# Performance work log

Hardware: AMD Instinct MI355X
Metric: run time of the kernel (lower is better)

The kernel has to match this reference:

```python
import jax, jax.numpy as jnp
import numpy as np

B, N, D_MODEL, N_HEAD, D_FFN = 256, 128, 256, 8, 1024
HEAD_DIM = D_MODEL // N_HEAD


def layer_norm(x, g, b, eps=1e-5):
    mu = jnp.mean(x, axis=-1, keepdims=True)
    var = jnp.var(x, axis=-1, keepdims=True)
    return (x - mu) * jax.lax.rsqrt(var + eps) * g + b


def setup_inputs() -> dict:
    key = jax.random.key(0)
    ks = jax.random.split(key, 20)
    s = 0.02
    w = lambda k, shape: jax.random.normal(k, shape, jnp.float32) * s
    return {
        "node_embedding": jax.random.normal(ks[0], (B, N, D_MODEL), jnp.float32),
        "node_mask": jnp.ones((B, N), jnp.float32),
        "adjacency": (jax.random.uniform(ks[1], (B, N, N)) < 0.1).astype(jnp.float32),
        "distance": jax.random.uniform(ks[2], (B, N, N), jnp.float32) * 10.0,
        "Wq": w(ks[3], (D_MODEL, D_MODEL)), "bq": jnp.zeros((D_MODEL,), jnp.float32),
        "Wk": w(ks[4], (D_MODEL, D_MODEL)), "bk": jnp.zeros((D_MODEL,), jnp.float32),
        "Wv": w(ks[5], (D_MODEL, D_MODEL)), "bv": jnp.zeros((D_MODEL,), jnp.float32),
        "Wo": w(ks[6], (D_MODEL, D_MODEL)), "bo": jnp.zeros((D_MODEL,), jnp.float32),
        "ln1_g": jnp.ones((D_MODEL,), jnp.float32), "ln1_b": jnp.zeros((D_MODEL,), jnp.float32),
        "W1": w(ks[7], (D_MODEL, D_FFN)), "b1": jnp.zeros((D_FFN,), jnp.float32),
        "W2": w(ks[8], (D_FFN, D_MODEL)), "b2": jnp.zeros((D_MODEL,), jnp.float32),
        "ln2_g": jnp.ones((D_MODEL,), jnp.float32), "ln2_b": jnp.zeros((D_MODEL,), jnp.float32),
    }


def reference(node_embedding, node_mask, adjacency, distance,
              Wq, bq, Wk, bk, Wv, bv, Wo, bo,
              ln1_g, ln1_b, W1, b1, W2, b2, ln2_g, ln2_b):
    X = node_embedding  # (B, N, d)
    split = lambda t: t.reshape(B, N, N_HEAD, HEAD_DIM).transpose(0, 2, 1, 3)  # (B,H,N,hd)
    Q = split(X @ Wq + bq)
    K = split(X @ Wk + bk)
    V = split(X @ Wv + bv)
    scores = jnp.einsum("bhqd,bhkd->bhqk", Q, K) / jnp.sqrt(jnp.float32(HEAD_DIM))
    # graph-aware biases: adjacency + distance added per-head before softmax
    scores = scores + adjacency[:, None, :, :] + distance[:, None, :, :]
    # key-side padding mask
    scores = scores + (1.0 - node_mask)[:, None, None, :] * jnp.float32(-1e9)
    attn = jax.nn.softmax(scores, axis=-1)  # (B,H,N,N)
    ctx = jnp.einsum("bhqk,bhkd->bhqd", attn, V).transpose(0, 2, 1, 3).reshape(B, N, D_MODEL)
    Y = ctx @ Wo + bo
    X = X + layer_norm(Y, ln1_g, ln1_b)  # pre-LN AddNorm (dropout=0, eval)
    H = jax.nn.gelu(X @ W1 + b1)
    Y = H @ W2 + b2
    X = X + layer_norm(Y, ln2_g, ln2_b)
    return X, attn
```

## Files before the change

### kernel.cpp

```cpp
#include <hip/hip_runtime.h>
#include <hip/hip_bf16.h>
#include <type_traits>


typedef __bf16 bf16x8 __attribute__((ext_vector_type(8)));
typedef float f32x4 __attribute__((ext_vector_type(4)));

__device__ __forceinline__ float gelu_tanh(float x) {
    float x3 = x * x * x;
    float t = tanhf(0.7978845608028654f * (x + 0.044715f * x3));
    return 0.5f * x * (1.0f + t);
}

__global__ __launch_bounds__(256) void prep_kernel(
    const float* __restrict__ Wq, const float* __restrict__ Wk,
    const float* __restrict__ Wv, const float* __restrict__ Wo,
    const float* __restrict__ W1, const float* __restrict__ W2,
    const float* __restrict__ bq, const float* __restrict__ bk,
    const float* __restrict__ bv,
    __bf16* __restrict__ WqkvT, __bf16* __restrict__ WoT,
    __bf16* __restrict__ W1T, __bf16* __restrict__ W2T,
    float* __restrict__ bqkv)
{
    int id = blockIdx.x * 256 + threadIdx.x;
    if (id < 196608) {
        int n = id >> 8, k = id & 255;
        float v = (n < 256) ? Wq[k * 256 + n]
                : (n < 512) ? Wk[k * 256 + (n - 256)]
                            : Wv[k * 256 + (n - 512)];
        WqkvT[n * 256 + k] = (__bf16)v;
    } else if (id < 262144) {
        int loc = id - 196608; int n = loc >> 8, k = loc & 255;
        WoT[n * 256 + k] = (__bf16)Wo[k * 256 + n];
    } else if (id < 524288) {
        int loc = id - 262144; int n = loc >> 8, k = loc & 255;
        W1T[n * 256 + k] = (__bf16)W1[k * 1024 + n];
    } else if (id < 786432) {
        int loc = id - 524288; int n = loc >> 10, k = loc & 1023;
        W2T[n * 1024 + k] = (__bf16)W2[k * 256 + n];
    } else if (id < 787200) {
        int i = id - 786432;
        bqkv[i] = (i < 256) ? bq[i] : (i < 512) ? bk[i - 256] : bv[i - 512];
    }
}

template <typename TA, int EPI>
__global__ __launch_bounds__(256) void gemm_kernel(
    const TA* __restrict__ A, const __bf16* __restrict__ Bt,
    const float* __restrict__ bias, void* __restrict__ outp,
    int M, int N, int K)
{
    __shared__ __bf16 As[128][40];
    __shared__ __bf16 Bs[128][40];
    const int t = threadIdx.x;
    const int w = t >> 6, l = t & 63;
    const int wr = w >> 1, wc = w & 1;
    const int lr = l & 15, lg = l >> 4;
    const int bm = blockIdx.y * 128, bn = blockIdx.x * 128;
    const int srow = t >> 1, sc0 = (t & 1) * 16;

    f32x4 acc[4][4];
#pragma unroll
    for (int m = 0; m < 4; m++)
#pragma unroll
        for (int n = 0; n < 4; n++) acc[m][n] = (f32x4){0.f, 0.f, 0.f, 0.f};

    for (int k0 = 0; k0 < K; k0 += 32) {
        if constexpr (std::is_same<TA, float>::value) {
            const float* ap = A + (size_t)(bm + srow) * K + k0 + sc0;
            __bf16 tmp[16];
#pragma unroll
            for (int i = 0; i < 16; i += 4) {
                float4 f = *(const float4*)(ap + i);
                tmp[i] = (__bf16)f.x; tmp[i + 1] = (__bf16)f.y;
                tmp[i + 2] = (__bf16)f.z; tmp[i + 3] = (__bf16)f.w;
            }
            *(bf16x8*)&As[srow][sc0]     = *(bf16x8*)&tmp[0];
            *(bf16x8*)&As[srow][sc0 + 8] = *(bf16x8*)&tmp[8];
        } else {
            const __bf16* ap = A + (size_t)(bm + srow) * K + k0 + sc0;
            *(bf16x8*)&As[srow][sc0]     = *(const bf16x8*)(ap);
            *(bf16x8*)&As[srow][sc0 + 8] = *(const bf16x8*)(ap + 8);
        }
        {
            const __bf16* bp = Bt + (size_t)(bn + srow) * K + k0 + sc0;
            *(bf16x8*)&Bs[srow][sc0]     = *(const bf16x8*)(bp);
            *(bf16x8*)&Bs[srow][sc0 + 8] = *(const bf16x8*)(bp + 8);
        }
        __syncthreads();
        bf16x8 af[4], bfr[4];
#pragma unroll
        for (int m = 0; m < 4; m++)
            af[m] = *(bf16x8*)&As[wr * 64 + m * 16 + lr][lg * 8];
#pragma unroll
        for (int n = 0; n < 4; n++)
            bfr[n] = *(bf16x8*)&Bs[wc * 64 + n * 16 + lr][lg * 8];
#pragma unroll
        for (int m = 0; m < 4; m++)
#pragma unroll
            for (int n = 0; n < 4; n++)
                acc[m][n] = __builtin_amdgcn_mfma_f32_16x16x32_bf16(
                    af[m], bfr[n], acc[m][n], 0, 0, 0);
        __syncthreads();
    }

#pragma unroll
    for (int n = 0; n < 4; n++) {
        const int col = bn + wc * 64 + n * 16 + lr;
        const float bv = bias[col];
#pragma unroll
        for (int m = 0; m < 4; m++) {
#pragma unroll
            for (int r = 0; r < 4; r++) {
                const int row = bm + wr * 64 + m * 16 + lg * 4 + r;
                float v = acc[m][n][r] + bv;
                if constexpr (EPI == 0)
                    ((float*)outp)[(size_t)row * N + col] = v;
                else if constexpr (EPI == 1)
                    ((__bf16*)outp)[(size_t)row * N + col] = (__bf16)v;
                else
                    ((__bf16*)outp)[(size_t)row * N + col] = (__bf16)gelu_tanh(v);
            }
        }
    }
}

__global__ __launch_bounds__(256) void attn_kernel(
    const __bf16* __restrict__ QKVb,
    const float* __restrict__ adj, const float* __restrict__ dist,
    const float* __restrict__ mask,
    float* __restrict__ attn_out,
    __bf16* __restrict__ ctx)
{
    __shared__ __bf16 Qs[128][40], Ks[128][40];
    __shared__ __bf16 Vt[32][136];
    __shared__ __bf16 Ps[128][136];
    const int bh = blockIdx.x, b = bh >> 3, h = bh & 7;
    const int t = threadIdx.x;
    const int w = t >> 6, l = t & 63;
    const int lr = l & 15, lg = l >> 4;
    {
        const int n = t >> 1, half = t & 1;
        const __bf16* base = QKVb + (size_t)(b * 128 + n) * 768 + h * 32 + half * 16;
        *(bf16x8*)&Qs[n][half * 16]     = *(const bf16x8*)(base);
        *(bf16x8*)&Qs[n][half * 16 + 8] = *(const bf16x8*)(base + 8);
        *(bf16x8*)&Ks[n][half * 16]     = *(const bf16x8*)(base + 256);
        *(bf16x8*)&Ks[n][half * 16 + 8] = *(const bf16x8*)(base + 256 + 8);
        bf16x8 v0 = *(const bf16x8*)(base + 512);
        bf16x8 v1 = *(const bf16x8*)(base + 512 + 8);
#pragma unroll
        for (int i = 0; i < 8; i++) Vt[half * 16 + i][n] = v0[i];
#pragma unroll
        for (int i = 0; i < 8; i++) Vt[half * 16 + 8 + i][n] = v1[i];
    }
    __syncthreads();

    f32x4 s[2][8];
    bf16x8 aq[2];
#pragma unroll
    for (int mt = 0; mt < 2; mt++)
        aq[mt] = *(bf16x8*)&Qs[w * 32 + mt * 16 + lr][lg * 8];
#pragma unroll
    for (int nt = 0; nt < 8; nt++) {
        bf16x8 bk_ = *(bf16x8*)&Ks[nt * 16 + lr][lg * 8];
#pragma unroll
        for (int mt = 0; mt < 2; mt++)
            s[mt][nt] = __builtin_amdgcn_mfma_f32_16x16x32_bf16(
                aq[mt], bk_, (f32x4){0.f, 0.f, 0.f, 0.f}, 0, 0, 0);
    }
    const float scale = 0.17677669529663687f;
    const float* adjb  = adj  + (size_t)b * 16384;
    const float* distb = dist + (size_t)b * 16384;
    float ma[8];
#pragma unroll
    for (int nt = 0; nt < 8; nt++)
        ma[nt] = (1.0f - mask[b * 128 + nt * 16 + lr]) * -1e9f;
#pragma unroll
    for (int mt = 0; mt < 2; mt++)
#pragma unroll
        for (int nt = 0; nt < 8; nt++)
#pragma unroll
            for (int r = 0; r < 4; r++) {
                int i = w * 32 + mt * 16 + lg * 4 + r, j = nt * 16 + lr;
                s[mt][nt][r] = s[mt][nt][r] * scale + adjb[i * 128 + j] +
                               distb[i * 128 + j] + ma[nt];
            }
    float* attn_base = attn_out + (size_t)bh * 16384;
#pragma unroll
    for (int mt = 0; mt < 2; mt++) {
#pragma unroll
        for (int r = 0; r < 4; r++) {
            float mx = s[mt][0][r];
#pragma unroll
            for (int nt = 1; nt < 8; nt++) mx = fmaxf(mx, s[mt][nt][r]);
#pragma unroll
            for (int msk = 1; msk < 16; msk <<= 1)
                mx = fmaxf(mx, __shfl_xor(mx, msk, 64));
            float p[8], sum = 0.f;
#pragma unroll
            for (int nt = 0; nt < 8; nt++) {
                p[nt] = __expf(s[mt][nt][r] - mx);
                sum += p[nt];
            }
#pragma unroll
            for (int msk = 1; msk < 16; msk <<= 1)
                sum += __shfl_xor(sum, msk, 64);
            float rinv = 1.0f / sum;
            int i = w * 32 + mt * 16 + lg * 4 + r;
#pragma unroll
            for (int nt = 0; nt < 8; nt++) {
                float a_ = p[nt] * rinv;
                attn_base[(size_t)i * 128 + nt * 16 + lr] = a_;
                Ps[i][nt * 16 + lr] = (__bf16)a_;
            }
        }
    }
    __syncthreads();
    f32x4 c[2][2];
#pragma unroll
    for (int mt = 0; mt < 2; mt++)
#pragma unroll
        for (int n2 = 0; n2 < 2; n2++) c[mt][n2] = (f32x4){0.f, 0.f, 0.f, 0.f};
#pragma unroll
    for (int ks = 0; ks < 4; ks++) {
        bf16x8 ap[2], bv_[2];
#pragma unroll
        for (int mt = 0; mt < 2; mt++)
            ap[mt] = *(bf16x8*)&Ps[w * 32 + mt * 16 + lr][ks * 32 + lg * 8];
#pragma unroll
        for (int n2 = 0; n2 < 2; n2++)
            bv_[n2] = *(bf16x8*)&Vt[n2 * 16 + lr][ks * 32 + lg * 8];
#pragma unroll
        for (int mt = 0; mt < 2; mt++)
#pragma unroll
            for (int n2 = 0; n2 < 2; n2++)
                c[mt][n2] = __builtin_amdgcn_mfma_f32_16x16x32_bf16(
                    ap[mt], bv_[n2], c[mt][n2], 0, 0, 0);
    }
#pragma unroll
    for (int mt = 0; mt < 2; mt++)
#pragma unroll
        for (int n2 = 0; n2 < 2; n2++)
#pragma unroll
            for (int r = 0; r < 4; r++) {
                int i = w * 32 + mt * 16 + lg * 4 + r, d = n2 * 16 + lr;
                ctx[(size_t)(b * 128 + i) * 256 + h * 32 + d] = (__bf16)c[mt][n2][r];
            }
}

__global__ __launch_bounds__(256) void addnorm_kernel(
    const float* __restrict__ X, const float* __restrict__ Y,
    const float* __restrict__ g, const float* __restrict__ be,
    float* __restrict__ out)
{
    const int w = threadIdx.x >> 6, l = threadIdx.x & 63;
    const size_t row = (size_t)blockIdx.x * 4 + w;
    const float4 y = *(const float4*)&Y[row * 256 + l * 4];
    float s = y.x + y.y + y.z + y.w;
    float q = y.x * y.x + y.y * y.y + y.z * y.z + y.w * y.w;
#pragma unroll
    for (int m = 1; m < 64; m <<= 1) {
        s += __shfl_xor(s, m, 64);
        q += __shfl_xor(q, m, 64);
    }
    const float mean = s * (1.f / 256.f);
    const float rs = rsqrtf(q * (1.f / 256.f) - mean * mean + 1e-5f);
    const float4 x = *(const float4*)&X[row * 256 + l * 4];
    const float4 gg = *(const float4*)&g[l * 4];
    const float4 bb = *(const float4*)&be[l * 4];
    float4 o;
    o.x = x.x + (y.x - mean) * rs * gg.x + bb.x;
    o.y = x.y + (y.y - mean) * rs * gg.y + bb.y;
    o.z = x.z + (y.z - mean) * rs * gg.z + bb.z;
    o.w = x.w + (y.w - mean) * rs * gg.w + bb.w;
    *(float4*)&out[row * 256 + l * 4] = o;
}

extern "C" void kernel_launch(void* const* d_in, const int* in_sizes, int n_in,
                              void* d_out, int out_size, void* d_ws, size_t ws_size,
                              hipStream_t stream)
{
    const float* node_emb  = (const float*)d_in[0];
    const float* node_mask = (const float*)d_in[1];
    const float* adjacency = (const float*)d_in[2];
    const float* distance  = (const float*)d_in[3];
    const float* Wq = (const float*)d_in[4];
    const float* bq = (const float*)d_in[5];
    const float* Wk = (const float*)d_in[6];
    const float* bk = (const float*)d_in[7];
    const float* Wv = (const float*)d_in[8];
    const float* bv = (const float*)d_in[9];
    const float* Wo = (const float*)d_in[10];
    const float* bo = (const float*)d_in[11];
    const float* ln1g = (const float*)d_in[12];
    const float* ln1b = (const float*)d_in[13];
    const float* W1 = (const float*)d_in[14];
    const float* b1 = (const float*)d_in[15];
    const float* W2 = (const float*)d_in[16];
    const float* b2 = (const float*)d_in[17];
    const float* ln2g = (const float*)d_in[18];
    const float* ln2b = (const float*)d_in[19];

    char* ws = (char*)d_ws;
    __bf16* WqkvT = (__bf16*)(ws + 0);
    __bf16* WoT   = (__bf16*)(ws + 393216);
    __bf16* W1T   = (__bf16*)(ws + 524288);
    __bf16* W2T   = (__bf16*)(ws + 1048576);
    float*  bqkv  = (float*)(ws + 1572864);
    __bf16* QKVb  = (__bf16*)(ws + 1575936);
    __bf16* ctx   = (__bf16*)(ws + 51907584);
    float*  Yb    = (float*)(ws + 68684800);
    float*  X1    = (float*)(ws + 102239232);
    __bf16* Hb    = (__bf16*)(ws + 135793664);
    float*  Y2    = (float*)QKVb;

    float* Xout = (float*)d_out;
    float* attn_out = Xout + (size_t)256 * 128 * 256;

    prep_kernel<<<3075, 256, 0, stream>>>(Wq, Wk, Wv, Wo, W1, W2, bq, bk, bv,
                                          WqkvT, WoT, W1T, W2T, bqkv);
    gemm_kernel<float, 1><<<dim3(6, 256), 256, 0, stream>>>(
        node_emb, WqkvT, bqkv, QKVb, 32768, 768, 256);
    attn_kernel<<<2048, 256, 0, stream>>>(QKVb, adjacency, distance, node_mask,
                                          attn_out, ctx);
    gemm_kernel<__bf16, 0><<<dim3(2, 256), 256, 0, stream>>>(
        ctx, WoT, bo, Yb, 32768, 256, 256);
    addnorm_kernel<<<8192, 256, 0, stream>>>(node_emb, Yb, ln1g, ln1b, X1);
    gemm_kernel<float, 2><<<dim3(8, 256), 256, 0, stream>>>(
        X1, W1T, b1, Hb, 32768, 1024, 256);
    gemm_kernel<__bf16, 0><<<dim3(2, 256), 256, 0, stream>>>(
        Hb, W2T, b2, Y2, 32768, 256, 1024);
    addnorm_kernel<<<8192, 256, 0, stream>>>(X1, Y2, ln2g, ln2b, Xout);
}
```

Baseline: 507.7 us.

## Widen GEMM N-tile, batch attention heads per block, pre-cast activations to bf16

Several ideas land together. The GEMM tile grows to 128x256 with launch_bounds(256,2), and the A operand is always bf16: node embeddings are cast in the prep kernel, and the first addnorm now also writes a bf16 copy of X1. The attention kernel moves to one 512-thread block per batch that loops over the 8 heads, so the adjacency+distance+mask bias is loaded into registers once per batch instead of once per head. The aim is to cut the repeated bias reads and the fp32 A-operand conversion inside GEMM, in exchange for extra cast passes, more registers per thread, and fewer attention blocks (256) on the GPU.

```diff
diff --git a/kernel.cpp b/kernel.cpp
--- a/kernel.cpp
+++ b/kernel.cpp
@@ -1,9 +1,9 @@
 #include <hip/hip_runtime.h>
 #include <hip/hip_bf16.h>
-#include <type_traits>
 
 
 typedef __bf16 bf16x8 __attribute__((ext_vector_type(8)));
+typedef __bf16 bf16x4 __attribute__((ext_vector_type(4)));
 typedef float f32x4 __attribute__((ext_vector_type(4)));
 
 __device__ __forceinline__ float gelu_tanh(float x) {
@@ -17,10 +17,10 @@
     const float* __restrict__ Wv, const float* __restrict__ Wo,
     const float* __restrict__ W1, const float* __restrict__ W2,
     const float* __restrict__ bq, const float* __restrict__ bk,
-    const float* __restrict__ bv,
+    const float* __restrict__ bv, const float* __restrict__ X0,
     __bf16* __restrict__ WqkvT, __bf16* __restrict__ WoT,
     __bf16* __restrict__ W1T, __bf16* __restrict__ W2T,
-    float* __restrict__ bqkv)
+    float* __restrict__ bqkv, __bf16* __restrict__ X0b)
 {
     int id = blockIdx.x * 256 + threadIdx.x;
     if (id < 196608) {
@@ -41,72 +41,66 @@
     } else if (id < 787200) {
         int i = id - 786432;
         bqkv[i] = (i < 256) ? bq[i] : (i < 512) ? bk[i - 256] : bv[i - 512];
-    }
-}
-
-template <typename TA, int EPI>
-__global__ __launch_bounds__(256) void gemm_kernel(
-    const TA* __restrict__ A, const __bf16* __restrict__ Bt,
+    } else {
+        int i = id - 787200;
+        X0b[i] = (__bf16)X0[i];
+    }
+}
+
+template <int EPI>
+__global__ __launch_bounds__(256, 2) void gemm_kernel(
+    const __bf16* __restrict__ A, const __bf16* __restrict__ Bt,
     const float* __restrict__ bias, void* __restrict__ outp,
     int M, int N, int K)
 {
     __shared__ __bf16 As[128][40];
-    __shared__ __bf16 Bs[128][40];
+    __shared__ __bf16 Bs[256][40];
     const int t = threadIdx.x;
     const int w = t >> 6, l = t & 63;
     const int wr = w >> 1, wc = w & 1;
     const int lr = l & 15, lg = l >> 4;
-    const int bm = blockIdx.y * 128, bn = blockIdx.x * 128;
-    const int srow = t >> 1, sc0 = (t & 1) * 16;
-
-    f32x4 acc[4][4];
+    const int bm = blockIdx.y * 128, bn = blockIdx.x * 256;
+    const int arow = t >> 1, ac0 = (t & 1) * 16;
+
+    f32x4 acc[4][8];
 #pragma unroll
     for (int m = 0; m < 4; m++)
 #pragma unroll
-        for (int n = 0; n < 4; n++) acc[m][n] = (f32x4){0.f, 0.f, 0.f, 0.f};
+        for (int n = 0; n < 8; n++) acc[m][n] = (f32x4){0.f, 0.f, 0.f, 0.f};
 
     for (int k0 = 0; k0 < K; k0 += 32) {
-        if constexpr (std::is_same<TA, float>::value) {
-            const float* ap = A + (size_t)(bm + srow) * K + k0 + sc0;
-            __bf16 tmp[16];
-#pragma unroll
-            for (int i = 0; i < 16; i += 4) {
-                float4 f = *(const float4*)(ap + i);
-                tmp[i] = (__bf16)f.x; tmp[i + 1] = (__bf16)f.y;
-                tmp[i + 2] = (__bf16)f.z; tmp[i + 3] = (__bf16)f.w;
-            }
-            *(bf16x8*)&As[srow][sc0]     = *(bf16x8*)&tmp[0];
-            *(bf16x8*)&As[srow][sc0 + 8] = *(bf16x8*)&tmp[8];
-        } else {
-            const __bf16* ap = A + (size_t)(bm + srow) * K + k0 + sc0;
-            *(bf16x8*)&As[srow][sc0]     = *(const bf16x8*)(ap);
-            *(bf16x8*)&As[srow][sc0 + 8] = *(const bf16x8*)(ap + 8);
-        }
         {
-            const __bf16* bp = Bt + (size_t)(bn + srow) * K + k0 + sc0;
-            *(bf16x8*)&Bs[srow][sc0]     = *(const bf16x8*)(bp);
-            *(bf16x8*)&Bs[srow][sc0 + 8] = *(const bf16x8*)(bp + 8);
-        }
-        __syncthreads();
-        bf16x8 af[4], bfr[4];
+            const __bf16* ap = A + (size_t)(bm + arow) * K + k0 + ac0;
+            *(bf16x8*)&As[arow][ac0]     = *(const bf16x8*)(ap);
+            *(bf16x8*)&As[arow][ac0 + 8] = *(const bf16x8*)(ap + 8);
+        }
+        {
+            const __bf16* bp = Bt + (size_t)(bn + t) * K + k0;
+            *(bf16x8*)&Bs[t][0]  = *(const bf16x8*)(bp);
+            *(bf16x8*)&Bs[t][8]  = *(const bf16x8*)(bp + 8);
+            *(bf16x8*)&Bs[t][16] = *(const bf16x8*)(bp + 16);
+            *(bf16x8*)&Bs[t][24] = *(const bf16x8*)(bp + 24);
+        }
+        __syncthreads();
+        bf16x8 af[4], bf_[8];
 #pragma unroll
         for (int m = 0; m < 4; m++)
             af[m] = *(bf16x8*)&As[wr * 64 + m * 16 + lr][lg * 8];
 #pragma unroll
-        for (int n = 0; n < 4; n++)
-            bfr[n] = *(bf16x8*)&Bs[wc * 64 + n * 16 + lr][lg * 8];
+        for (int n = 0; n < 8; n++)
+            bf_[n] = *(bf16x8*)&Bs[wc * 128 + n * 16 + lr][lg * 8];
 #pragma unroll
         for (int m = 0; m < 4; m++)
 #pragma unroll
-            for (int n = 0; n < 4; n++)
+            for (int n = 0; n < 8; n++)
                 acc[m][n] = __builtin_amdgcn_mfma_f32_16x16x32_bf16(
-                    af[m], bfr[n], acc[m][n], 0, 0, 0);
-        __syncthreads();
-    }
-
-#pragma unroll
-    for (int n = 0; n < 4; n++) {
-        const int col = bn + wc * 64 + n * 16 + lr;
+                    af[m], bf_[n], acc[m][n], 0, 0, 0);
+        __syncthreads();
+    }
+
+#pragma unroll
+    for (int n = 0; n < 8; n++) {
+        const int col = bn + wc * 128 + n * 16 + lr;
         const float bv = bias[col];
 #pragma unroll
         for (int m = 0; m < 4; m++) {
@@ -125,7 +119,7 @@
     }
 }
 
-__global__ __launch_bounds__(256) void attn_kernel(
+__global__ __launch_bounds__(512) void attn_kernel(
     const __bf16* __restrict__ QKVb,
     const float* __restrict__ adj, const float* __restrict__ dist,
     const float* __restrict__ mask,
@@ -135,78 +129,71 @@
     __shared__ __bf16 Qs[128][40], Ks[128][40];
     __shared__ __bf16 Vt[32][136];
     __shared__ __bf16 Ps[128][136];
-    const int bh = blockIdx.x, b = bh >> 3, h = bh & 7;
+    const int b = blockIdx.x;
     const int t = threadIdx.x;
     const int w = t >> 6, l = t & 63;
     const int lr = l & 15, lg = l >> 4;
-    {
-        const int n = t >> 1, half = t & 1;
-        const __bf16* base = QKVb + (size_t)(b * 128 + n) * 768 + h * 32 + half * 16;
-        *(bf16x8*)&Qs[n][half * 16]     = *(const bf16x8*)(base);
-        *(bf16x8*)&Qs[n][half * 16 + 8] = *(const bf16x8*)(base + 8);
-        *(bf16x8*)&Ks[n][half * 16]     = *(const bf16x8*)(base + 256);
-        *(bf16x8*)&Ks[n][half * 16 + 8] = *(const bf16x8*)(base + 256 + 8);
-        bf16x8 v0 = *(const bf16x8*)(base + 512);
-        bf16x8 v1 = *(const bf16x8*)(base + 512 + 8);
-#pragma unroll
-        for (int i = 0; i < 8; i++) Vt[half * 16 + i][n] = v0[i];
-#pragma unroll
-        for (int i = 0; i < 8; i++) Vt[half * 16 + 8 + i][n] = v1[i];
-    }
-    __syncthreads();
-
-    f32x4 s[2][8];
-    bf16x8 aq[2];
-#pragma unroll
-    for (int mt = 0; mt < 2; mt++)
-        aq[mt] = *(bf16x8*)&Qs[w * 32 + mt * 16 + lr][lg * 8];
-#pragma unroll
-    for (int nt = 0; nt < 8; nt++) {
-        bf16x8 bk_ = *(bf16x8*)&Ks[nt * 16 + lr][lg * 8];
-#pragma unroll
-        for (int mt = 0; mt < 2; mt++)
-            s[mt][nt] = __builtin_amdgcn_mfma_f32_16x16x32_bf16(
-                aq[mt], bk_, (f32x4){0.f, 0.f, 0.f, 0.f}, 0, 0, 0);
-    }
-    const float scale = 0.17677669529663687f;
+
     const float* adjb  = adj  + (size_t)b * 16384;
     const float* distb = dist + (size_t)b * 16384;
-    float ma[8];
-#pragma unroll
-    for (int nt = 0; nt < 8; nt++)
-        ma[nt] = (1.0f - mask[b * 128 + nt * 16 + lr]) * -1e9f;
-#pragma unroll
-    for (int mt = 0; mt < 2; mt++)
+    float breg[8][4];
+#pragma unroll
+    for (int nt = 0; nt < 8; nt++) {
+        const int j = nt * 16 + lr;
+        const float madd = (1.0f - mask[b * 128 + j]) * -1e9f;
+#pragma unroll
+        for (int r = 0; r < 4; r++) {
+            const int i = w * 16 + lg * 4 + r;
+            breg[nt][r] = adjb[i * 128 + j] + distb[i * 128 + j] + madd;
+        }
+    }
+
+    const int srow = t >> 2, sq = (t & 3) * 8;
+    const __bf16* qkvrow = QKVb + (size_t)(b * 128 + srow) * 768 + sq;
+    const float scale = 0.17677669529663687f;
+
+    for (int h = 0; h < 8; h++) {
+        *(bf16x8*)&Qs[srow][sq] = *(const bf16x8*)(qkvrow + h * 32);
+        *(bf16x8*)&Ks[srow][sq] = *(const bf16x8*)(qkvrow + h * 32 + 256);
+        bf16x8 v8 = *(const bf16x8*)(qkvrow + h * 32 + 512);
+#pragma unroll
+        for (int i2 = 0; i2 < 8; i2++) Vt[sq + i2][srow] = v8[i2];
+        __syncthreads();
+
+        bf16x8 aq = *(bf16x8*)&Qs[w * 16 + lr][lg * 8];
+        f32x4 s[8];
+#pragma unroll
+        for (int nt = 0; nt < 8; nt++) {
+            bf16x8 bk_ = *(bf16x8*)&Ks[nt * 16 + lr][lg * 8];
+            s[nt] = __builtin_amdgcn_mfma_f32_16x16x32_bf16(
+                aq, bk_, (f32x4){0.f, 0.f, 0.f, 0.f}, 0, 0, 0);
+        }
 #pragma unroll
         for (int nt = 0; nt < 8; nt++)
 #pragma unroll
-            for (int r = 0; r < 4; r++) {
-                int i = w * 32 + mt * 16 + lg * 4 + r, j = nt * 16 + lr;
-                s[mt][nt][r] = s[mt][nt][r] * scale + adjb[i * 128 + j] +
-                               distb[i * 128 + j] + ma[nt];
-            }
-    float* attn_base = attn_out + (size_t)bh * 16384;
-#pragma unroll
-    for (int mt = 0; mt < 2; mt++) {
+            for (int r = 0; r < 4; r++)
+                s[nt][r] = s[nt][r] * scale + breg[nt][r];
+
+        float* attn_base = attn_out + (size_t)(b * 8 + h) * 16384;
 #pragma unroll
         for (int r = 0; r < 4; r++) {
-            float mx = s[mt][0][r];
-#pragma unroll
-            for (int nt = 1; nt < 8; nt++) mx = fmaxf(mx, s[mt][nt][r]);
+            float mx = s[0][r];
+#pragma unroll
+            for (int nt = 1; nt < 8; nt++) mx = fmaxf(mx, s[nt][r]);
 #pragma unroll
             for (int msk = 1; msk < 16; msk <<= 1)
                 mx = fmaxf(mx, __shfl_xor(mx, msk, 64));
             float p[8], sum = 0.f;
 #pragma unroll
             for (int nt = 0; nt < 8; nt++) {
-                p[nt] = __expf(s[mt][nt][r] - mx);
+                p[nt] = __expf(s[nt][r] - mx);
                 sum += p[nt];
             }
 #pragma unroll
             for (int msk = 1; msk < 16; msk <<= 1)
                 sum += __shfl_xor(sum, msk, 64);
-            float rinv = 1.0f / sum;
-            int i = w * 32 + mt * 16 + lg * 4 + r;
+            const float rinv = 1.0f / sum;
+            const int i = w * 16 + lg * 4 + r;
 #pragma unroll
             for (int nt = 0; nt < 8; nt++) {
                 float a_ = p[nt] * rinv;
@@ -214,44 +201,37 @@
                 Ps[i][nt * 16 + lr] = (__bf16)a_;
             }
         }
-    }
-    __syncthreads();
-    f32x4 c[2][2];
-#pragma unroll
-    for (int mt = 0; mt < 2; mt++)
-#pragma unroll
-        for (int n2 = 0; n2 < 2; n2++) c[mt][n2] = (f32x4){0.f, 0.f, 0.f, 0.f};
-#pragma unroll
-    for (int ks = 0; ks < 4; ks++) {
-        bf16x8 ap[2], bv_[2];
-#pragma unroll
-        for (int mt = 0; mt < 2; mt++)
-            ap[mt] = *(bf16x8*)&Ps[w * 32 + mt * 16 + lr][ks * 32 + lg * 8];
+        __syncthreads();
+
+        f32x4 c[2];
+        c[0] = (f32x4){0.f, 0.f, 0.f, 0.f};
+        c[1] = (f32x4){0.f, 0.f, 0.f, 0.f};
+#pragma unroll
+        for (int ks = 0; ks < 4; ks++) {
+            bf16x8 ap = *(bf16x8*)&Ps[w * 16 + lr][ks * 32 + lg * 8];
+#pragma unroll
+            for (int n2 = 0; n2 < 2; n2++) {
+                bf16x8 bv_ = *(bf16x8*)&Vt[n2 * 16 + lr][ks * 32 + lg * 8];
+                c[n2] = __builtin_amdgcn_mfma_f32_16x16x32_bf16(
+                    ap, bv_, c[n2], 0, 0, 0);
+            }
+        }
 #pragma unroll
         for (int n2 = 0; n2 < 2; n2++)
-            bv_[n2] = *(bf16x8*)&Vt[n2 * 16 + lr][ks * 32 + lg * 8];
-#pragma unroll
-        for (int mt = 0; mt < 2; mt++)
-#pragma unroll
-            for (int n2 = 0; n2 < 2; n2++)
-                c[mt][n2] = __builtin_amdgcn_mfma_f32_16x16x32_bf16(
-                    ap[mt], bv_[n2], c[mt][n2], 0, 0, 0);
-    }
-#pragma unroll
-    for (int mt = 0; mt < 2; mt++)
-#pragma unroll
-        for (int n2 = 0; n2 < 2; n2++)
 #pragma unroll
             for (int r = 0; r < 4; r++) {
-                int i = w * 32 + mt * 16 + lg * 4 + r, d = n2 * 16 + lr;
-                ctx[(size_t)(b * 128 + i) * 256 + h * 32 + d] = (__bf16)c[mt][n2][r];
-            }
-}
-
+                const int i = w * 16 + lg * 4 + r, d = n2 * 16 + lr;
+                ctx[(size_t)(b * 128 + i) * 256 + h * 32 + d] = (__bf16)c[n2][r];
+            }
+        __syncthreads();
+    }
+}
+
+template <bool WRITE_BF16>
 __global__ __launch_bounds__(256) void addnorm_kernel(
     const float* __restrict__ X, const float* __restrict__ Y,
     const float* __restrict__ g, const float* __restrict__ be,
-    float* __restrict__ out)
+    float* __restrict__ out, __bf16* __restrict__ outb)
 {
     const int w = threadIdx.x >> 6, l = threadIdx.x & 63;
     const size_t row = (size_t)blockIdx.x * 4 + w;
@@ -274,6 +254,12 @@
     o.z = x.z + (y.z - mean) * rs * gg.z + bb.z;
     o.w = x.w + (y.w - mean) * rs * gg.w + bb.w;
     *(float4*)&out[row * 256 + l * 4] = o;
+    if constexpr (WRITE_BF16) {
+        bf16x4 ob;
+        ob[0] = (__bf16)o.x; ob[1] = (__bf16)o.y;
+        ob[2] = (__bf16)o.z; ob[3] = (__bf16)o.w;
+        *(bf16x4*)&outb[row * 256 + l * 4] = ob;
+    }
 }
 
 extern "C" void kernel_launch(void* const* d_in, const int* in_sizes, int n_in,
@@ -307,28 +293,33 @@
     __bf16* W1T   = (__bf16*)(ws + 524288);
     __bf16* W2T   = (__bf16*)(ws + 1048576);
     float*  bqkv  = (float*)(ws + 1572864);
-    __bf16* QKVb  = (__bf16*)(ws + 1575936);
-    __bf16* ctx   = (__bf16*)(ws + 51907584);
-    float*  Yb    = (float*)(ws + 68684800);
-    float*  X1    = (float*)(ws + 102239232);
-    __bf16* Hb    = (__bf16*)(ws + 135793664);
+    __bf16* X0b   = (__bf16*)(ws + 1575936);
+    __bf16* QKVb  = (__bf16*)(ws + 18353152);
+    __bf16* ctx   = (__bf16*)(ws + 68684800);
+    float*  Yb    = (float*)(ws + 85462016);
+    float*  X1    = (float*)(ws + 119016448);
+    __bf16* X1b   = (__bf16*)(ws + 152570880);
+    __bf16* Hb    = (__bf16*)(ws + 169348096);
     float*  Y2    = (float*)QKVb;
 
     float* Xout = (float*)d_out;
     float* attn_out = Xout + (size_t)256 * 128 * 256;
 
-    prep_kernel<<<3075, 256, 0, stream>>>(Wq, Wk, Wv, Wo, W1, W2, bq, bk, bv,
-                                          WqkvT, WoT, W1T, W2T, bqkv);
-    gemm_kernel<float, 1><<<dim3(6, 256), 256, 0, stream>>>(
-        node_emb, WqkvT, bqkv, QKVb, 32768, 768, 256);
-    attn_kernel<<<2048, 256, 0, stream>>>(QKVb, adjacency, distance, node_mask,
-                                          attn_out, ctx);
-    gemm_kernel<__bf16, 0><<<dim3(2, 256), 256, 0, stream>>>(
+    prep_kernel<<<35843, 256, 0, stream>>>(Wq, Wk, Wv, Wo, W1, W2, bq, bk, bv,
+                                           node_emb, WqkvT, WoT, W1T, W2T,
+                                           bqkv, X0b);
+    gemm_kernel<1><<<dim3(3, 256), 256, 0, stream>>>(
+        X0b, WqkvT, bqkv, QKVb, 32768, 768, 256);
+    attn_kernel<<<256, 512, 0, stream>>>(QKVb, adjacency, distance, node_mask,
+                                         attn_out, ctx);
+    gemm_kernel<0><<<dim3(1, 256), 256, 0, stream>>>(
         ctx, WoT, bo, Yb, 32768, 256, 256);
-    addnorm_kernel<<<8192, 256, 0, stream>>>(node_emb, Yb, ln1g, ln1b, X1);
-    gemm_kernel<float, 2><<<dim3(8, 256), 256, 0, stream>>>(
-        X1, W1T, b1, Hb, 32768, 1024, 256);
-    gemm_kernel<__bf16, 0><<<dim3(2, 256), 256, 0, stream>>>(
+    addnorm_kernel<true><<<8192, 256, 0, stream>>>(node_emb, Yb, ln1g, ln1b,
+                                                   X1, X1b);
+    gemm_kernel<2><<<dim3(4, 256), 256, 0, stream>>>(
+        X1b, W1T, b1, Hb, 32768, 1024, 256);
+    gemm_kernel<0><<<dim3(1, 256), 256, 0, stream>>>(
         Hb, W2T, b2, Y2, 32768, 256, 1024);
-    addnorm_kernel<<<8192, 256, 0, stream>>>(X1, Y2, ln2g, ln2b, Xout);
-}
+    addnorm_kernel<false><<<8192, 256, 0, stream>>>(X1, Y2, ln2g, ln2b,
+                                                    Xout, nullptr);
+}
```

Result: no change. 503.1 us (-0.9%).
